# Performance work log

Hardware: AMD Instinct MI355X
Metric: run time of the kernel (lower is better)

Reference implementation:

```python
import jax, jax.numpy as jnp
import numpy as np

GAUSS_START = 0.5
GAUSS_END = 5.0
N_GAUSS = 16
N_ATOMS = 3072
N_GRAPHS = 64
K_GRID = 4096


def setup_inputs() -> dict:
    key = jax.random.key(0)
    k1, k2, k3, k4 = jax.random.split(key, 4)
    coeff = jax.random.normal(k1, (N_ATOMS, N_GAUSS), dtype=jnp.float32)
    atom_coord = jax.random.normal(k2, (N_ATOMS, 3), dtype=jnp.float32)
    grid = jax.random.normal(k3, (N_GRAPHS, K_GRID, 3), dtype=jnp.float32)
    batch = jnp.sort(jax.random.randint(k4, (N_ATOMS,), 0, N_GRAPHS, dtype=jnp.int64))
    return {"coeff": coeff, "atom_coord": atom_coord, "grid": grid, "batch": batch}


def reference(coeff, atom_coord, grid, batch):
    # Precomputed gaussian widths (buffers in the torch module)
    sigma = jnp.linspace(GAUSS_START, GAUSS_END, N_GAUSS, dtype=jnp.float32)
    sigma_r = 1.0 / (sigma * np.float32(np.sqrt(2.0 * np.pi))) ** 3  # (n_gauss,)
    sigma_2r = 1.0 / sigma ** 2  # (n_gauss,)

    # Gather per-atom grid: (N, K, 3)
    sample_vec = grid[batch] - atom_coord[:, None, :]
    r2 = jnp.sum(sample_vec ** 2, axis=-1)  # (N, K)
    # Gaussian basis on grid: (N, K, n_gauss)
    orbital = jnp.exp(-r2[..., None] * sigma_2r) * sigma_r
    # Weighted sum over gaussians: (N, K)
    density = jnp.einsum('nkg,ng->nk', orbital, coeff)
    # Scatter-add atoms back to their graph: (G, K)
    return jax.ops.segment_sum(density, batch, num_segments=N_GRAPHS)
```

## Files before the change

kernel.cpp:

```cpp
#include <hip/hip_runtime.h>
#include <cmath>

constexpr int N_GAUSS = 16;
constexpr int N_GRAPHS = 64;
constexpr int K_GRID = 4096;

constexpr int NSEG = 512;
constexpr int TSTRIDE = 528;
constexpr float RMAX = 12.0f;

constexpr int KCHUNK = 256;
constexpr int KPER = 4;
constexpr int KSPAN = KCHUNK * KPER;
constexpr int CHUNKS = K_GRID / KSPAN;
constexpr int APB = 12;

struct GaussParams {
    float ns2[N_GAUSS];
    float b[N_GAUSS];
};

__device__ __forceinline__ float fast_exp2(float x) {
    return __builtin_amdgcn_exp2f(x);
}

__global__ __launch_bounds__(256) void build_table_kernel(
    const float* __restrict__ coeff,
    float* __restrict__ table,
    float* __restrict__ out,
    GaussParams p)
{
    const int a = blockIdx.y;
    const int t = (int)threadIdx.x;
    const int n = blockIdx.x * 256 + t;

    if (blockIdx.x == 0 && a < (N_GRAPHS * K_GRID) / (256 * 4)) {
        ((float4*)out)[a * 256 + t] = make_float4(0.f, 0.f, 0.f, 0.f);
    }

    const float* __restrict__ cf = coeff + a * N_GAUSS;

    auto eval = [&](int idx) -> float {
        if (idx > NSEG) return 0.f;
        const float r = (float)idx * (RMAX / (float)NSEG);
        const float r2 = r * r;
        float a0 = 0.f, a1 = 0.f, a2 = 0.f, a3 = 0.f;
        #pragma unroll
        for (int g = 0; g < N_GAUSS; g += 4) {
            a0 = fmaf(cf[g + 0], fast_exp2(fmaf(r2, p.ns2[g + 0], p.b[g + 0])), a0);
            a1 = fmaf(cf[g + 1], fast_exp2(fmaf(r2, p.ns2[g + 1], p.b[g + 1])), a1);
            a2 = fmaf(cf[g + 2], fast_exp2(fmaf(r2, p.ns2[g + 2], p.b[g + 2])), a2);
            a3 = fmaf(cf[g + 3], fast_exp2(fmaf(r2, p.ns2[g + 3], p.b[g + 3])), a3);
        }
        return (a0 + a1) + (a2 + a3);
    };

    table[(size_t)a * TSTRIDE + n] = eval(n);
    if (blockIdx.x == 1 && t < TSTRIDE - 512) {
        const int n2 = 512 + t;
        table[(size_t)a * TSTRIDE + n2] = eval(n2);
    }
}

__global__ __launch_bounds__(KCHUNK) void GaussianOrbital_kernel(
    const float* __restrict__ table,
    const float* __restrict__ atom_coord,
    const float* __restrict__ grid,
    const int* __restrict__ batch,
    float* __restrict__ out,
    int n_atoms)
{
    __shared__ float lds[APB * TSTRIDE];

    const int chunk = blockIdx.x;
    const int ablk  = blockIdx.y;
    const int t = (int)threadIdx.x;

    const int lo = ablk * APB;
    int hi = lo + APB; if (hi > n_atoms) hi = n_atoms;

    {
        const float4* __restrict__ src = (const float4*)(table + (size_t)lo * TSTRIDE);
        float4* dst = (float4*)lds;
        const int nvec = (hi - lo) * TSTRIDE / 4;
        #pragma unroll 2
        for (int i = t; i < nvec; i += KCHUNK) dst[i] = src[i];
    }
    __syncthreads();

    int cur_g = __builtin_amdgcn_readfirstlane(batch[lo]);

    float kx[KPER], ky[KPER], kz[KPER], acc[KPER];
    auto load_grid = [&](int g) {
        #pragma unroll
        for (int j = 0; j < KPER; ++j) {
            const int k = chunk * KSPAN + j * KCHUNK + t;
            const int b = (g * K_GRID + k) * 3;
            kx[j] = grid[b + 0]; ky[j] = grid[b + 1]; kz[j] = grid[b + 2];
        }
    };
    auto flush = [&](int g) {
        #pragma unroll
        for (int j = 0; j < KPER; ++j) {
            const int k = chunk * KSPAN + j * KCHUNK + t;
            atomicAdd(&out[g * K_GRID + k], acc[j]);
            acc[j] = 0.f;
        }
    };
    load_grid(cur_g);
    #pragma unroll
    for (int j = 0; j < KPER; ++j) acc[j] = 0.f;

    for (int a = lo; a < hi; ++a) {
        const int g = __builtin_amdgcn_readfirstlane(batch[a]);
        if (g != cur_g) {
            flush(cur_g);
            cur_g = g;
            load_grid(cur_g);
        }

        const float ax = atom_coord[a * 3 + 0];
        const float ay = atom_coord[a * 3 + 1];
        const float az = atom_coord[a * 3 + 2];
        const float* __restrict__ T = lds + (a - lo) * TSTRIDE;

        float fr[KPER]; int ii[KPER];
        #pragma unroll
        for (int j = 0; j < KPER; ++j) {
            const float dx = kx[j] - ax, dy = ky[j] - ay, dz = kz[j] - az;
            const float r2 = fmaf(dx, dx, fmaf(dy, dy, dz * dz));
            float tt = __builtin_amdgcn_sqrtf(r2) * ((float)NSEG / RMAX);
            tt = fminf(tt, (float)(NSEG - 1));
            const int i = (int)tt;
            fr[j] = tt - (float)i;
            ii[j] = i;
        }
        float f0[KPER], f1[KPER];
        #pragma unroll
        for (int j = 0; j < KPER; ++j) { f0[j] = T[ii[j]]; f1[j] = T[ii[j] + 1]; }
        #pragma unroll
        for (int j = 0; j < KPER; ++j) acc[j] = acc[j] + fmaf(fr[j], f1[j] - f0[j], f0[j]);
    }

    flush(cur_g);
}

extern "C" void kernel_launch(void* const* d_in, const int* in_sizes, int n_in,
                              void* d_out, int out_size, void* d_ws, size_t ws_size,
                              hipStream_t stream)
{
    const float* coeff      = (const float*)d_in[0];
    const float* atom_coord = (const float*)d_in[1];
    const float* grid       = (const float*)d_in[2];
    const int*   batch      = (const int*)d_in[3];
    float* out   = (float*)d_out;
    float* table = (float*)d_ws;
    const int n_atoms = in_sizes[0] / N_GAUSS;

    GaussParams p;
    const double sqrt2pi = 2.50662827463100050242;
    for (int g = 0; g < N_GAUSS; ++g) {
        const double sigma = 0.5 + (5.0 - 0.5) * (double)g / (double)(N_GAUSS - 1);
        p.ns2[g] = (float)(-1.44269504088896340736 / (sigma * sigma));
        const double sr = 1.0 / (sigma * sqrt2pi * sigma * sqrt2pi * sigma * sqrt2pi);
        p.b[g] = (float)(std::log2(sr));
    }

    {
        dim3 gDim(2, n_atoms);
        hipLaunchKernelGGL(build_table_kernel, gDim, dim3(256), 0, stream,
                           coeff, table, out, p);
    }
    {
        const int n_ablk = (n_atoms + APB - 1) / APB;
        dim3 gDim(CHUNKS, n_ablk);
        hipLaunchKernelGGL(GaussianOrbital_kernel, gDim, dim3(KCHUNK), 0, stream,
                           table, atom_coord, grid, batch, out, n_atoms);
    }
}
```

Baseline: 81.74 us.

## Fuse radial table build into main kernel LDS and double per-thread grid points

Removes the separate table-building kernel and its global workspace round trip. Each block now evaluates the per-atom radial lookup table directly into shared memory, and a small kernel zeroes the output instead. KPER rises from 4 to 8, which halves the number of chunks, so each block's table build is amortised over twice as many grid points. The cost is that every chunk recomputes the tables (2 chunks now instead of one global build), and the larger KPER lowers block-level parallelism.

```diff
diff --git a/kernel.cpp b/kernel.cpp
--- a/kernel.cpp
+++ b/kernel.cpp
@@ -10,7 +10,7 @@
 constexpr float RMAX = 12.0f;
 
 constexpr int KCHUNK = 256;
-constexpr int KPER = 4;
+constexpr int KPER = 8;
 constexpr int KSPAN = KCHUNK * KPER;
 constexpr int CHUNKS = K_GRID / KSPAN;
 constexpr int APB = 12;
@@ -24,51 +24,17 @@
     return __builtin_amdgcn_exp2f(x);
 }
 
-__global__ __launch_bounds__(256) void build_table_kernel(
-    const float* __restrict__ coeff,
-    float* __restrict__ table,
-    float* __restrict__ out,
-    GaussParams p)
-{
-    const int a = blockIdx.y;
-    const int t = (int)threadIdx.x;
-    const int n = blockIdx.x * 256 + t;
-
-    if (blockIdx.x == 0 && a < (N_GRAPHS * K_GRID) / (256 * 4)) {
-        ((float4*)out)[a * 256 + t] = make_float4(0.f, 0.f, 0.f, 0.f);
-    }
-
-    const float* __restrict__ cf = coeff + a * N_GAUSS;
-
-    auto eval = [&](int idx) -> float {
-        if (idx > NSEG) return 0.f;
-        const float r = (float)idx * (RMAX / (float)NSEG);
-        const float r2 = r * r;
-        float a0 = 0.f, a1 = 0.f, a2 = 0.f, a3 = 0.f;
-        #pragma unroll
-        for (int g = 0; g < N_GAUSS; g += 4) {
-            a0 = fmaf(cf[g + 0], fast_exp2(fmaf(r2, p.ns2[g + 0], p.b[g + 0])), a0);
-            a1 = fmaf(cf[g + 1], fast_exp2(fmaf(r2, p.ns2[g + 1], p.b[g + 1])), a1);
-            a2 = fmaf(cf[g + 2], fast_exp2(fmaf(r2, p.ns2[g + 2], p.b[g + 2])), a2);
-            a3 = fmaf(cf[g + 3], fast_exp2(fmaf(r2, p.ns2[g + 3], p.b[g + 3])), a3);
-        }
-        return (a0 + a1) + (a2 + a3);
-    };
-
-    table[(size_t)a * TSTRIDE + n] = eval(n);
-    if (blockIdx.x == 1 && t < TSTRIDE - 512) {
-        const int n2 = 512 + t;
-        table[(size_t)a * TSTRIDE + n2] = eval(n2);
-    }
+__global__ __launch_bounds__(256) void zero_out_kernel(float4* __restrict__ out4) {
+    out4[blockIdx.x * 256 + threadIdx.x] = make_float4(0.f, 0.f, 0.f, 0.f);
 }
 
 __global__ __launch_bounds__(KCHUNK) void GaussianOrbital_kernel(
-    const float* __restrict__ table,
+    const float* __restrict__ coeff,
     const float* __restrict__ atom_coord,
     const float* __restrict__ grid,
     const int* __restrict__ batch,
     float* __restrict__ out,
-    int n_atoms)
+    GaussParams p, int n_atoms)
 {
     __shared__ float lds[APB * TSTRIDE];
 
@@ -79,12 +45,22 @@
     const int lo = ablk * APB;
     int hi = lo + APB; if (hi > n_atoms) hi = n_atoms;
 
-    {
-        const float4* __restrict__ src = (const float4*)(table + (size_t)lo * TSTRIDE);
-        float4* dst = (float4*)lds;
-        const int nvec = (hi - lo) * TSTRIDE / 4;
-        #pragma unroll 2
-        for (int i = t; i < nvec; i += KCHUNK) dst[i] = src[i];
+    for (int a = lo; a < hi; ++a) {
+        const float* __restrict__ cf = coeff + a * N_GAUSS;
+        float* __restrict__ T = lds + (a - lo) * TSTRIDE;
+        for (int e = t; e <= NSEG; e += KCHUNK) {
+            const float r = (float)e * (RMAX / (float)NSEG);
+            const float r2 = r * r;
+            float a0 = 0.f, a1 = 0.f, a2 = 0.f, a3 = 0.f;
+            #pragma unroll
+            for (int g = 0; g < N_GAUSS; g += 4) {
+                a0 = fmaf(cf[g + 0], fast_exp2(fmaf(r2, p.ns2[g + 0], p.b[g + 0])), a0);
+                a1 = fmaf(cf[g + 1], fast_exp2(fmaf(r2, p.ns2[g + 1], p.b[g + 1])), a1);
+                a2 = fmaf(cf[g + 2], fast_exp2(fmaf(r2, p.ns2[g + 2], p.b[g + 2])), a2);
+                a3 = fmaf(cf[g + 3], fast_exp2(fmaf(r2, p.ns2[g + 3], p.b[g + 3])), a3);
+            }
+            T[e] = (a0 + a1) + (a2 + a3);
+        }
     }
     __syncthreads();
 
@@ -153,8 +129,7 @@
     const float* atom_coord = (const float*)d_in[1];
     const float* grid       = (const float*)d_in[2];
     const int*   batch      = (const int*)d_in[3];
-    float* out   = (float*)d_out;
-    float* table = (float*)d_ws;
+    float* out = (float*)d_out;
     const int n_atoms = in_sizes[0] / N_GAUSS;
 
     GaussParams p;
@@ -167,14 +142,14 @@
     }
 
     {
-        dim3 gDim(2, n_atoms);
-        hipLaunchKernelGGL(build_table_kernel, gDim, dim3(256), 0, stream,
-                           coeff, table, out, p);
+        const int nvec4 = (N_GRAPHS * K_GRID) / 4;
+        hipLaunchKernelGGL(zero_out_kernel, dim3(nvec4 / 256), dim3(256), 0, stream,
+                           (float4*)out);
     }
     {
         const int n_ablk = (n_atoms + APB - 1) / APB;
         dim3 gDim(CHUNKS, n_ablk);
         hipLaunchKernelGGL(GaussianOrbital_kernel, gDim, dim3(KCHUNK), 0, stream,
-                           table, atom_coord, grid, batch, out, n_atoms);
+                           coeff, atom_coord, grid, batch, out, p, n_atoms);
     }
 }
```

After: 82.92 us. About the same (+1.5%).
